# Performance work log

Hardware: AMD Instinct MI355X
Metric: run time of the kernel (lower is better)

The kernel has to match this reference:

```python
import jax, jax.numpy as jnp
import numpy as np

N_NODES = 10000
N_EDGES = 80000
F_IN = 128
H1 = 2048
H2 = 2048
H3 = 1024


def _sgconv(x, pos, src, dst, W_in, b_in, W_out, b_out):
    # geo-GCN SpatialGraphConv with hidden_size=1:
    # message(j->i) = relu(Linear(pos_j - pos_i)) * x_j ; aggr='add' ; then Linear out
    rel = pos[src] - pos[dst]                      # [E, 2]  (pos_j - pos_i)
    scale = jax.nn.relu(rel @ W_in + b_in)         # [E, C_in]
    msg = scale * x[src]                           # [E, C_in]
    agg = jax.ops.segment_sum(msg, dst, num_segments=x.shape[0])  # [N, C_in]
    return agg @ W_out + b_out                     # [N, C_out]


def setup_inputs() -> dict:
    key = jax.random.key(0)
    ks = jax.random.split(key, 12)
    x = jax.random.normal(ks[0], (N_NODES, F_IN), dtype=jnp.float32)
    pos = jax.random.normal(ks[1], (N_NODES, 2), dtype=jnp.float32)
    edge_index = jax.random.randint(ks[2], (2, N_EDGES), 0, N_NODES, dtype=jnp.int32)

    def lin(k, fan_in, fan_out):
        lim = 1.0 / np.sqrt(fan_in)
        kw, kb = jax.random.split(k)
        W = jax.random.uniform(kw, (fan_in, fan_out), jnp.float32, -lim, lim)
        b = jax.random.uniform(kb, (fan_out,), jnp.float32, -lim, lim)
        return W, b

    W_in1, b_in1 = lin(ks[3], 2, F_IN)
    W_out1, b_out1 = lin(ks[4], F_IN, H1)
    W_in2, b_in2 = lin(ks[5], 2, H1)
    W_out2, b_out2 = lin(ks[6], H1, H2)
    W_in3, b_in3 = lin(ks[7], 2, H2)
    W_out3, b_out3 = lin(ks[8], H2, H3)

    return {
        "x": x, "pos": pos, "edge_index": edge_index,
        "W_in1": W_in1, "b_in1": b_in1, "W_out1": W_out1, "b_out1": b_out1,
        "W_in2": W_in2, "b_in2": b_in2, "W_out2": W_out2, "b_out2": b_out2,
        "W_in3": W_in3, "b_in3": b_in3, "W_out3": W_out3, "b_out3": b_out3,
    }


def reference(x, pos, edge_index,
              W_in1, b_in1, W_out1, b_out1,
              W_in2, b_in2, W_out2, b_out2,
              W_in3, b_in3, W_out3, b_out3):
    src, dst = edge_index[0], edge_index[1]  # flow source_to_target: j=src, i=dst
    h = jax.nn.relu(_sgconv(x, pos, src, dst, W_in1, b_in1, W_out1, b_out1))
    h = jax.nn.relu(_sgconv(h, pos, src, dst, W_in2, b_in2, W_out2, b_out2))
    h = jax.nn.relu(_sgconv(h, pos, src, dst, W_in3, b_in3, W_out3, b_out3))
    # F.normalize(h, dim=1): L2 normalize rows with eps clamp 1e-12
    norm = jnp.linalg.norm(h, axis=1, keepdims=True)
    return h / jnp.maximum(norm, 1e-12)
```

## Files before the change

### kernel.cpp

```cpp
#include <hip/hip_runtime.h>
#include <hip/hip_bf16.h>

#define DEVI __device__ __forceinline__

constexpr int NN = 10000;
constexpr int NE = 80000;
constexpr int AGG_ROWS = 10240;

typedef __attribute__((ext_vector_type(8))) short bf16x8;
typedef __attribute__((ext_vector_type(4))) float f32x4;

DEVI float blo(unsigned int u) {
  union { unsigned int i; float f; } c; c.i = u << 16; return c.f;
}
DEVI float bhi(unsigned int u) {
  union { unsigned int i; float f; } c; c.i = u & 0xffff0000u; return c.f;
}
DEVI unsigned short f2b(float f) {
  union { float f; unsigned int i; } c; c.f = f;
  unsigned int i = c.i;
  return (unsigned short)((i + 0x7fffu + ((i >> 16) & 1u)) >> 16);
}
DEVI void st1(float* p, float v) { *p = v; }
DEVI void st1(unsigned short* p, float v) { *p = f2b(v); }
DEVI void store8b(unsigned short* p, const float v[8]) {
  int4 pk;
  pk.x = (int)((unsigned)f2b(v[0]) | ((unsigned)f2b(v[1]) << 16));
  pk.y = (int)((unsigned)f2b(v[2]) | ((unsigned)f2b(v[3]) << 16));
  pk.z = (int)((unsigned)f2b(v[4]) | ((unsigned)f2b(v[5]) << 16));
  pk.w = (int)((unsigned)f2b(v[6]) | ((unsigned)f2b(v[7]) << 16));
  *reinterpret_cast<int4*>(p) = pk;
}

DEVI void gload16(const void* g, void* l) {
  __builtin_amdgcn_global_load_lds(
      (const __attribute__((address_space(1))) void*)g,
      (__attribute__((address_space(3))) void*)l, 16, 0, 0);
}

__global__ __launch_bounds__(256)
void hist_kernel(const int* __restrict__ dst, int* __restrict__ cnt) {
  int e = blockIdx.x * 256 + threadIdx.x;
  if (e < NE) atomicAdd(&cnt[dst[e]], 1);
}

__global__ __launch_bounds__(256)
void scan_kernel(const int* __restrict__ cnt, int* __restrict__ off,
                 int* __restrict__ cursor) {
  __shared__ int buf[256];
  __shared__ int carry;
  if (threadIdx.x == 0) carry = 0;
  __syncthreads();
  for (int base = 0; base < NN; base += 256) {
    int i = base + threadIdx.x;
    int v = (i < NN) ? cnt[i] : 0;
    buf[threadIdx.x] = v;
    __syncthreads();
#pragma unroll
    for (int o = 1; o < 256; o <<= 1) {
      int t = (threadIdx.x >= o) ? buf[threadIdx.x - o] : 0;
      __syncthreads();
      buf[threadIdx.x] += t;
      __syncthreads();
    }
    int incl = buf[threadIdx.x];
    int c0 = carry;
    if (i < NN) { int ex = c0 + incl - v; off[i] = ex; cursor[i] = ex; }
    __syncthreads();
    if (threadIdx.x == 255) carry = c0 + incl;
    __syncthreads();
  }
}

__global__ __launch_bounds__(256)
void bucket_kernel(const int* __restrict__ src, const int* __restrict__ dst,
                   int* __restrict__ cursor, int* __restrict__ es) {
  int e = blockIdx.x * 256 + threadIdx.x;
  if (e < NE) {
    int p = atomicAdd(&cursor[dst[e]], 1);
    es[p] = src[e];
  }
}

__global__ __launch_bounds__(256)
void transpose_w(const float* __restrict__ W, unsigned short* __restrict__ WT,
                 int K, int N) {
  __shared__ float tile[32][33];
  int tx = threadIdx.x & 31, ty = threadIdx.x >> 5;
  int n0 = blockIdx.x * 32, k0 = blockIdx.y * 32;
#pragma unroll
  for (int j = 0; j < 32; j += 8)
    tile[ty + j][tx] = W[(size_t)(k0 + ty + j) * N + n0 + tx];
  __syncthreads();
#pragma unroll
  for (int j = 0; j < 32; j += 8)
    WT[(size_t)(n0 + ty + j) * K + k0 + tx] = f2b(tile[tx][ty + j]);
}

__global__ __launch_bounds__(256)
void gather_l1(const float* __restrict__ x, const float* __restrict__ pos,
               const int* __restrict__ off, const int* __restrict__ cnt,
               const int* __restrict__ es,
               const float* __restrict__ Win, const float* __restrict__ bin,
               unsigned short* __restrict__ agg) {
  constexpr int C = 128;
  int lane = threadIdx.x & 63;
  int i = blockIdx.x * 4 + (threadIdx.x >> 6);
  if (i >= NN) return;
  int c = lane * 2;
  float w00 = Win[c], w01 = Win[c + 1];
  float w10 = Win[C + c], w11 = Win[C + c + 1];
  float b0 = bin[c], b1 = bin[c + 1];
  float a0 = 0.f, a1 = 0.f;
  float2 pd = *reinterpret_cast<const float2*>(pos + 2 * i);
  int s0 = off[i], n = cnt[i];

  float2 r0, r1, r2, r3, q0, q1, q2, q3;
  auto ld = [&](int k, float2& r, float2& q) {
    if (k < n) {
      int s = es[s0 + k];
      float2 ps = *reinterpret_cast<const float2*>(pos + 2 * s);
      r = make_float2(ps.x - pd.x, ps.y - pd.y);
      q = *reinterpret_cast<const float2*>(x + (size_t)s * C + c);
    }
  };
  auto fma1 = [&](const float2& r, const float2& q) {
    float sc0 = fmaxf(fmaf(r.x, w00, fmaf(r.y, w10, b0)), 0.f);
    float sc1 = fmaxf(fmaf(r.x, w01, fmaf(r.y, w11, b1)), 0.f);
    a0 = fmaf(sc0, q.x, a0);
    a1 = fmaf(sc1, q.y, a1);
  };
  ld(0, r0, q0); ld(1, r1, q1); ld(2, r2, q2); ld(3, r3, q3);
  for (int k = 0; k < n; k += 4) {
    fma1(r0, q0); ld(k + 4, r0, q0);
    if (k + 1 < n) { fma1(r1, q1); } ld(k + 5, r1, q1);
    if (k + 2 < n) { fma1(r2, q2); } ld(k + 6, r2, q2);
    if (k + 3 < n) { fma1(r3, q3); } ld(k + 7, r3, q3);
  }
  unsigned int pk = (unsigned)f2b(a0) | ((unsigned)f2b(a1) << 16);
  *reinterpret_cast<unsigned int*>(agg + (size_t)i * C + c) = pk;
}

__global__ __launch_bounds__(256)
void gather_c2048(const unsigned short* __restrict__ x, const float* __restrict__ pos,
                  const int* __restrict__ off, const int* __restrict__ cnt,
                  const int* __restrict__ es,
                  const float* __restrict__ Win, const float* __restrict__ bin,
                  unsigned short* __restrict__ agg) {
  constexpr int C = 2048;
  constexpr int V = 8;
  int i = blockIdx.x;
  int c = threadIdx.x * V;
  float w0[V], w1[V], bb[V], acc[V];
#pragma unroll
  for (int j = 0; j < V; ++j) {
    w0[j] = Win[c + j]; w1[j] = Win[C + c + j]; bb[j] = bin[c + j]; acc[j] = 0.f;
  }
  float2 pd = *reinterpret_cast<const float2*>(pos + 2 * i);
  int s0 = off[i], n = cnt[i];

  float2 r0, r1, r2, r3;
  int4 q0, q1, q2, q3;
  auto ld = [&](int k, float2& r, int4& q) {
    if (k < n) {
      int s = es[s0 + k];
      float2 ps = *reinterpret_cast<const float2*>(pos + 2 * s);
      r = make_float2(ps.x - pd.x, ps.y - pd.y);
      q = *reinterpret_cast<const int4*>(x + (size_t)s * C + c);
    }
  };
  auto fma8 = [&](const float2& r, const int4& q) {
    float xv[V] = { blo(q.x), bhi(q.x), blo(q.y), bhi(q.y),
                    blo(q.z), bhi(q.z), blo(q.w), bhi(q.w) };
#pragma unroll
    for (int j = 0; j < V; ++j) {
      float sc = fmaxf(fmaf(r.x, w0[j], fmaf(r.y, w1[j], bb[j])), 0.f);
      acc[j] = fmaf(sc, xv[j], acc[j]);
    }
  };
  ld(0, r0, q0); ld(1, r1, q1); ld(2, r2, q2); ld(3, r3, q3);
  for (int k = 0; k < n; k += 4) {
    fma8(r0, q0); ld(k + 4, r0, q0);
    if (k + 1 < n) { fma8(r1, q1); } ld(k + 5, r1, q1);
    if (k + 2 < n) { fma8(r2, q2); } ld(k + 6, r2, q2);
    if (k + 3 < n) { fma8(r3, q3); } ld(k + 7, r3, q3);
  }
  store8b(agg + (size_t)i * C + c, acc);
}

template <typename OT>
__global__ __launch_bounds__(256, 2)
void gemm160(const unsigned short* __restrict__ A,
             const unsigned short* __restrict__ BT,
             const float* __restrict__ bias, OT* __restrict__ out,
             int M, int N, int K) {
  extern __shared__ unsigned short lds[];
  const int t = threadIdx.x;
  const int lane = t & 63, wid = t >> 6;
  const int wr = wid >> 1, wc = wid & 1;

  const int nwg = gridDim.x * gridDim.y;
  const int orig = blockIdx.y * gridDim.x + blockIdx.x;
  const int swz = (orig & 7) * (nwg >> 3) + (orig >> 3);
  const int bx = swz % gridDim.x, by = swz / gridDim.x;
  const int m0 = by * 160, n0 = bx * 128;
  const int nk = K >> 6;

  const int lrow = lane >> 3;
  const int schunk = (lane & 7) ^ lrow;
  const unsigned short* gA = A + (size_t)(m0 + wid * 40 + lrow) * K + schunk * 8;
  const unsigned short* gB = BT + (size_t)(n0 + wid * 32 + lrow) * K + schunk * 8;
  unsigned short* lA = lds + (wid * 5) * 512 + lane * 8;
  unsigned short* lB = lds + 20480 + (wid * 4) * 512 + lane * 8;

  auto STAGE = [&](int buf, int kt) {
    const size_t ko = (size_t)kt << 6;
#pragma unroll
    for (int jj = 0; jj < 5; ++jj)
      gload16(gA + (size_t)(jj * 8) * K + ko, lA + buf * 10240 + jj * 512);
#pragma unroll
    for (int jj = 0; jj < 4; ++jj)
      gload16(gB + (size_t)(jj * 8) * K + ko, lB + buf * 8192 + jj * 512);
  };

  const int frow = lane & 15;
  const int fr7 = frow & 7;
  const int slot0 = ((lane >> 4) ^ fr7) * 8;
  const int slot1 = ((4 + (lane >> 4)) ^ fr7) * 8;
  const int paRow = (wr * 80 + frow) * 64;
  const int pbRow = (wc * 64 + frow) * 64;

  f32x4 acc[5][4];
#pragma unroll
  for (int m = 0; m < 5; ++m)
#pragma unroll
    for (int n = 0; n < 4; ++n) acc[m][n] = 0.f;

  STAGE(0, 0);

  int cur = 0;
  for (int kt = 0; kt < nk; ++kt) {
    if (kt + 1 < nk) {
      STAGE(cur ^ 1, kt + 1);
      asm volatile("s_waitcnt vmcnt(9)" ::: "memory");
    } else {
      asm volatile("s_waitcnt vmcnt(0)" ::: "memory");
    }
    asm volatile("s_barrier" ::: "memory");
    const unsigned short* pa = lds + cur * 10240 + paRow;
    const unsigned short* pb = lds + 20480 + cur * 8192 + pbRow;
#pragma unroll
    for (int ks = 0; ks < 2; ++ks) {
      const int sl = ks ? slot1 : slot0;
      bf16x8 af[5], bf[4];
#pragma unroll
      for (int m = 0; m < 5; ++m)
        af[m] = *reinterpret_cast<const bf16x8*>(pa + m * 1024 + sl);
#pragma unroll
      for (int n = 0; n < 4; ++n)
        bf[n] = *reinterpret_cast<const bf16x8*>(pb + n * 1024 + sl);
      __builtin_amdgcn_s_setprio(1);
#pragma unroll
      for (int m = 0; m < 5; ++m)
#pragma unroll
        for (int n = 0; n < 4; ++n)
          acc[m][n] = __builtin_amdgcn_mfma_f32_16x16x32_bf16(
              af[m], bf[n], acc[m][n], 0, 0, 0);
      __builtin_amdgcn_s_setprio(0);
    }
    asm volatile("s_barrier" ::: "memory");
    cur ^= 1;
  }

  const int ccol = lane & 15;
  const int crow = (lane >> 4) * 4;
  float bv[4];
#pragma unroll
  for (int n = 0; n < 4; ++n)
    bv[n] = bias[n0 + wc * 64 + n * 16 + ccol];
#pragma unroll
  for (int m = 0; m < 5; ++m) {
    int gm0 = m0 + wr * 80 + m * 16 + crow;
#pragma unroll
    for (int r = 0; r < 4; ++r) {
      int gm = gm0 + r;
      if (gm < M) {
        size_t base = (size_t)gm * N + n0 + wc * 64 + ccol;
#pragma unroll
        for (int n = 0; n < 4; ++n)
          st1(out + base + n * 16, fmaxf(acc[m][n][r] + bv[n], 0.f));
      }
    }
  }
}

__global__ __launch_bounds__(256)
void l2norm_kernel(float* __restrict__ out) {
  constexpr int C = 1024;
  float* p = out + (size_t)blockIdx.x * C;
  float4 v = *reinterpret_cast<const float4*>(p + threadIdx.x * 4);
  float s = v.x * v.x + v.y * v.y + v.z * v.z + v.w * v.w;
#pragma unroll
  for (int o = 32; o > 0; o >>= 1) s += __shfl_down(s, o);
  __shared__ float wsum[4];
  if ((threadIdx.x & 63) == 0) wsum[threadIdx.x >> 6] = s;
  __syncthreads();
  float tot = wsum[0] + wsum[1] + wsum[2] + wsum[3];
  float inv = 1.0f / fmaxf(sqrtf(tot), 1e-12f);
  float4 r = make_float4(v.x * inv, v.y * inv, v.z * inv, v.w * inv);
  *reinterpret_cast<float4*>(p + threadIdx.x * 4) = r;
}

extern "C" void kernel_launch(void* const* d_in, const int* in_sizes, int n_in,
                              void* d_out, int out_size, void* d_ws, size_t ws_size,
                              hipStream_t stream) {
  (void)in_sizes; (void)n_in; (void)out_size; (void)ws_size;
  const float* x     = (const float*)d_in[0];
  const float* pos   = (const float*)d_in[1];
  const int*   ei    = (const int*)d_in[2];
  const int*   srcv  = ei;
  const int*   dstv  = ei + NE;
  const float* Win1  = (const float*)d_in[3];
  const float* bin1  = (const float*)d_in[4];
  const float* Wout1 = (const float*)d_in[5];
  const float* bout1 = (const float*)d_in[6];
  const float* Win2  = (const float*)d_in[7];
  const float* bin2  = (const float*)d_in[8];
  const float* Wout2 = (const float*)d_in[9];
  const float* bout2 = (const float*)d_in[10];
  const float* Win3  = (const float*)d_in[11];
  const float* bin3  = (const float*)d_in[12];
  const float* Wout3 = (const float*)d_in[13];
  const float* bout3 = (const float*)d_in[14];
  float* outp = (float*)d_out;

  char* ws = (char*)d_ws;
  unsigned short* aggb = (unsigned short*)ws;
  unsigned short* h1   = (unsigned short*)(ws + 41943040);
  unsigned short* W2T  = (unsigned short*)(ws + 82903040);
  unsigned short* W3T  = (unsigned short*)(ws + 91291648);
  unsigned short* W1T  = (unsigned short*)(ws + 95485952);
  int* cnt    = (int*)(ws + 96010240);
  int* off    = (int*)(ws + 96050240);
  int* cursor = (int*)(ws + 96090240);
  int* es     = (int*)(ws + 96130240);
  unsigned short* h2 = (unsigned short*)d_out;

  hipFuncSetAttribute((const void*)gemm160<unsigned short>,
                      hipFuncAttributeMaxDynamicSharedMemorySize, 73728);
  hipFuncSetAttribute((const void*)gemm160<float>,
                      hipFuncAttributeMaxDynamicSharedMemorySize, 73728);

  const dim3 blk(256);
  const int eb = (NE + 255) / 256;

  hipMemsetAsync(cnt, 0, NN * sizeof(int), stream);
  hist_kernel<<<eb, blk, 0, stream>>>(dstv, cnt);
  scan_kernel<<<1, blk, 0, stream>>>(cnt, off, cursor);
  bucket_kernel<<<eb, blk, 0, stream>>>(srcv, dstv, cursor, es);

  transpose_w<<<dim3(2048 / 32, 128 / 32),  blk, 0, stream>>>(Wout1, W1T, 128, 2048);
  transpose_w<<<dim3(2048 / 32, 2048 / 32), blk, 0, stream>>>(Wout2, W2T, 2048, 2048);
  transpose_w<<<dim3(1024 / 32, 2048 / 32), blk, 0, stream>>>(Wout3, W3T, 2048, 1024);

  hipMemsetAsync(aggb + (size_t)NN * 2048, 0, (size_t)(AGG_ROWS - NN) * 2048 * 2, stream);

  gather_l1<<<(NN + 3) / 4, blk, 0, stream>>>(x, pos, off, cnt, es, Win1, bin1, aggb);
  gemm160<unsigned short><<<dim3(2048 / 128, AGG_ROWS / 160), blk, 73728, stream>>>(
      aggb, W1T, bout1, h1, NN, 2048, 128);

  gather_c2048<<<NN, blk, 0, stream>>>(h1, pos, off, cnt, es, Win2, bin2, aggb);
  gemm160<unsigned short><<<dim3(2048 / 128, AGG_ROWS / 160), blk, 73728, stream>>>(
      aggb, W2T, bout2, h2, NN, 2048, 2048);

  gather_c2048<<<NN, blk, 0, stream>>>(h2, pos, off, cnt, es, Win3, bin3, aggb);
  gemm160<float><<<dim3(1024 / 128, AGG_ROWS / 160), blk, 73728, stream>>>(
      aggb, W3T, bout3, outp, NN, 1024, 2048);

  l2norm_kernel<<<NN, blk, 0, stream>>>(outp);
}
```

Baseline: 347.3 us.

## Precompute packed edge records and split wide gathers into column chunks

The bucket kernel now writes one float4 per edge holding the relative position and the source index. This removes the per-edge pos lookups and subtractions from every gather pass. The 2048-wide gathers are restructured so each wave handles one node and a 128-column chunk with 2 columns per lane, ordered so that consecutive blocks cover the same column chunk across nearby nodes. Each lane now issues 4-byte loads instead of 16-byte loads, so the wide-gather path makes many more load instructions and edge-record reads. In exchange, the grid is larger and the column-chunk working set is more L2-friendly.

```diff
diff --git a/kernel.cpp b/kernel.cpp
--- a/kernel.cpp
+++ b/kernel.cpp
@@ -23,14 +23,6 @@
 }
 DEVI void st1(float* p, float v) { *p = v; }
 DEVI void st1(unsigned short* p, float v) { *p = f2b(v); }
-DEVI void store8b(unsigned short* p, const float v[8]) {
-  int4 pk;
-  pk.x = (int)((unsigned)f2b(v[0]) | ((unsigned)f2b(v[1]) << 16));
-  pk.y = (int)((unsigned)f2b(v[2]) | ((unsigned)f2b(v[3]) << 16));
-  pk.z = (int)((unsigned)f2b(v[4]) | ((unsigned)f2b(v[5]) << 16));
-  pk.w = (int)((unsigned)f2b(v[6]) | ((unsigned)f2b(v[7]) << 16));
-  *reinterpret_cast<int4*>(p) = pk;
-}
 
 DEVI void gload16(const void* g, void* l) {
   __builtin_amdgcn_global_load_lds(
@@ -74,11 +66,15 @@
 
 __global__ __launch_bounds__(256)
 void bucket_kernel(const int* __restrict__ src, const int* __restrict__ dst,
-                   int* __restrict__ cursor, int* __restrict__ es) {
+                   const float* __restrict__ pos,
+                   int* __restrict__ cursor, float4* __restrict__ epack) {
   int e = blockIdx.x * 256 + threadIdx.x;
   if (e < NE) {
-    int p = atomicAdd(&cursor[dst[e]], 1);
-    es[p] = src[e];
+    int s = src[e], d = dst[e];
+    int p = atomicAdd(&cursor[d], 1);
+    float2 ps = *reinterpret_cast<const float2*>(pos + 2 * s);
+    float2 pd = *reinterpret_cast<const float2*>(pos + 2 * d);
+    epack[p] = make_float4(ps.x - pd.x, ps.y - pd.y, __int_as_float(s), 0.f);
   }
 }
 
@@ -98,9 +94,9 @@
 }
 
 __global__ __launch_bounds__(256)
-void gather_l1(const float* __restrict__ x, const float* __restrict__ pos,
+void gather_l1(const float* __restrict__ x,
                const int* __restrict__ off, const int* __restrict__ cnt,
-               const int* __restrict__ es,
+               const float4* __restrict__ epack,
                const float* __restrict__ Win, const float* __restrict__ bin,
                unsigned short* __restrict__ agg) {
   constexpr int C = 128;
@@ -112,80 +108,80 @@
   float w10 = Win[C + c], w11 = Win[C + c + 1];
   float b0 = bin[c], b1 = bin[c + 1];
   float a0 = 0.f, a1 = 0.f;
-  float2 pd = *reinterpret_cast<const float2*>(pos + 2 * i);
   int s0 = off[i], n = cnt[i];
 
-  float2 r0, r1, r2, r3, q0, q1, q2, q3;
-  auto ld = [&](int k, float2& r, float2& q) {
+  float4 e0, e1, e2, e3;
+  float2 q0, q1, q2, q3;
+  auto ld = [&](int k, float4& e, float2& q) {
     if (k < n) {
-      int s = es[s0 + k];
-      float2 ps = *reinterpret_cast<const float2*>(pos + 2 * s);
-      r = make_float2(ps.x - pd.x, ps.y - pd.y);
+      e = epack[s0 + k];
+      int s = __float_as_int(e.z);
       q = *reinterpret_cast<const float2*>(x + (size_t)s * C + c);
     }
   };
-  auto fma1 = [&](const float2& r, const float2& q) {
-    float sc0 = fmaxf(fmaf(r.x, w00, fmaf(r.y, w10, b0)), 0.f);
-    float sc1 = fmaxf(fmaf(r.x, w01, fmaf(r.y, w11, b1)), 0.f);
+  auto acc1 = [&](const float4& e, const float2& q) {
+    float sc0 = fmaxf(fmaf(e.x, w00, fmaf(e.y, w10, b0)), 0.f);
+    float sc1 = fmaxf(fmaf(e.x, w01, fmaf(e.y, w11, b1)), 0.f);
     a0 = fmaf(sc0, q.x, a0);
     a1 = fmaf(sc1, q.y, a1);
   };
-  ld(0, r0, q0); ld(1, r1, q1); ld(2, r2, q2); ld(3, r3, q3);
+  ld(0, e0, q0); ld(1, e1, q1); ld(2, e2, q2); ld(3, e3, q3);
   for (int k = 0; k < n; k += 4) {
-    fma1(r0, q0); ld(k + 4, r0, q0);
-    if (k + 1 < n) { fma1(r1, q1); } ld(k + 5, r1, q1);
-    if (k + 2 < n) { fma1(r2, q2); } ld(k + 6, r2, q2);
-    if (k + 3 < n) { fma1(r3, q3); } ld(k + 7, r3, q3);
+    acc1(e0, q0); ld(k + 4, e0, q0);
+    if (k + 1 < n) { acc1(e1, q1); } ld(k + 5, e1, q1);
+    if (k + 2 < n) { acc1(e2, q2); } ld(k + 6, e2, q2);
+    if (k + 3 < n) { acc1(e3, q3); } ld(k + 7, e3, q3);
   }
   unsigned int pk = (unsigned)f2b(a0) | ((unsigned)f2b(a1) << 16);
   *reinterpret_cast<unsigned int*>(agg + (size_t)i * C + c) = pk;
 }
 
 __global__ __launch_bounds__(256)
-void gather_c2048(const unsigned short* __restrict__ x, const float* __restrict__ pos,
+void gather_chunk(const unsigned short* __restrict__ x,
                   const int* __restrict__ off, const int* __restrict__ cnt,
-                  const int* __restrict__ es,
+                  const float4* __restrict__ epack,
                   const float* __restrict__ Win, const float* __restrict__ bin,
-                  unsigned short* __restrict__ agg) {
+                  unsigned short* __restrict__ agg, int ngb8) {
   constexpr int C = 2048;
-  constexpr int V = 8;
-  int i = blockIdx.x;
-  int c = threadIdx.x * V;
-  float w0[V], w1[V], bb[V], acc[V];
-#pragma unroll
-  for (int j = 0; j < V; ++j) {
-    w0[j] = Win[c + j]; w1[j] = Win[C + c + j]; bb[j] = bin[c + j]; acc[j] = 0.f;
-  }
-  float2 pd = *reinterpret_cast<const float2*>(pos + 2 * i);
+  int wgid = blockIdx.x;
+  int half = wgid >= ngb8;
+  int base = half ? wgid - ngb8 : wgid;
+  int chunk = (base & 7) + (half << 3);
+  int grp = base >> 3;
+  int lane = threadIdx.x & 63;
+  int i = grp * 4 + (threadIdx.x >> 6);
+  if (i >= NN) return;
+  int c = chunk * 128 + lane * 2;
+  float w00 = Win[c], w01 = Win[c + 1];
+  float w10 = Win[C + c], w11 = Win[C + c + 1];
+  float b0 = bin[c], b1 = bin[c + 1];
+  float a0 = 0.f, a1 = 0.f;
   int s0 = off[i], n = cnt[i];
 
-  float2 r0, r1, r2, r3;
-  int4 q0, q1, q2, q3;
-  auto ld = [&](int k, float2& r, int4& q) {
+  float4 e0, e1, e2, e3;
+  unsigned int q0, q1, q2, q3;
+  auto ld = [&](int k, float4& e, unsigned int& q) {
     if (k < n) {
-      int s = es[s0 + k];
-      float2 ps = *reinterpret_cast<const float2*>(pos + 2 * s);
-      r = make_float2(ps.x - pd.x, ps.y - pd.y);
-      q = *reinterpret_cast<const int4*>(x + (size_t)s * C + c);
-    }
-  };
-  auto fma8 = [&](const float2& r, const int4& q) {
-    float xv[V] = { blo(q.x), bhi(q.x), blo(q.y), bhi(q.y),
-                    blo(q.z), bhi(q.z), blo(q.w), bhi(q.w) };
-#pragma unroll
-    for (int j = 0; j < V; ++j) {
-      float sc = fmaxf(fmaf(r.x, w0[j], fmaf(r.y, w1[j], bb[j])), 0.f);
-      acc[j] = fmaf(sc, xv[j], acc[j]);
-    }
-  };
-  ld(0, r0, q0); ld(1, r1, q1); ld(2, r2, q2); ld(3, r3, q3);
+      e = epack[s0 + k];
+      int s = __float_as_int(e.z);
+      q = *reinterpret_cast<const unsigned int*>(x + (size_t)s * C + c);
+    }
+  };
+  auto acc1 = [&](const float4& e, unsigned int q) {
+    float sc0 = fmaxf(fmaf(e.x, w00, fmaf(e.y, w10, b0)), 0.f);
+    float sc1 = fmaxf(fmaf(e.x, w01, fmaf(e.y, w11, b1)), 0.f);
+    a0 = fmaf(sc0, blo(q), a0);
+    a1 = fmaf(sc1, bhi(q), a1);
+  };
+  ld(0, e0, q0); ld(1, e1, q1); ld(2, e2, q2); ld(3, e3, q3);
   for (int k = 0; k < n; k += 4) {
-    fma8(r0, q0); ld(k + 4, r0, q0);
-    if (k + 1 < n) { fma8(r1, q1); } ld(k + 5, r1, q1);
-    if (k + 2 < n) { fma8(r2, q2); } ld(k + 6, r2, q2);
-    if (k + 3 < n) { fma8(r3, q3); } ld(k + 7, r3, q3);
-  }
-  store8b(agg + (size_t)i * C + c, acc);
+    acc1(e0, q0); ld(k + 4, e0, q0);
+    if (k + 1 < n) { acc1(e1, q1); } ld(k + 5, e1, q1);
+    if (k + 2 < n) { acc1(e2, q2); } ld(k + 6, e2, q2);
+    if (k + 3 < n) { acc1(e3, q3); } ld(k + 7, e3, q3);
+  }
+  unsigned int pk = (unsigned)f2b(a0) | ((unsigned)f2b(a1) << 16);
+  *reinterpret_cast<unsigned int*>(agg + (size_t)i * C + c) = pk;
 }
 
 template <typename OT>
@@ -343,7 +339,7 @@
   int* cnt    = (int*)(ws + 96010240);
   int* off    = (int*)(ws + 96050240);
   int* cursor = (int*)(ws + 96090240);
-  int* es     = (int*)(ws + 96130240);
+  float4* epack = (float4*)(ws + 96130240);
   unsigned short* h2 = (unsigned short*)d_out;
 
   hipFuncSetAttribute((const void*)gemm160<unsigned short>,
@@ -353,11 +349,12 @@
 
   const dim3 blk(256);
   const int eb = (NE + 255) / 256;
+  const int ngb8 = ((NN + 3) / 4) * 8;
 
   hipMemsetAsync(cnt, 0, NN * sizeof(int), stream);
   hist_kernel<<<eb, blk, 0, stream>>>(dstv, cnt);
   scan_kernel<<<1, blk, 0, stream>>>(cnt, off, cursor);
-  bucket_kernel<<<eb, blk, 0, stream>>>(srcv, dstv, cursor, es);
+  bucket_kernel<<<eb, blk, 0, stream>>>(srcv, dstv, pos, cursor, epack);
 
   transpose_w<<<dim3(2048 / 32, 128 / 32),  blk, 0, stream>>>(Wout1, W1T, 128, 2048);
   transpose_w<<<dim3(2048 / 32, 2048 / 32), blk, 0, stream>>>(Wout2, W2T, 2048, 2048);
@@ -365,15 +362,15 @@
 
   hipMemsetAsync(aggb + (size_t)NN * 2048, 0, (size_t)(AGG_ROWS - NN) * 2048 * 2, stream);
 
-  gather_l1<<<(NN + 3) / 4, blk, 0, stream>>>(x, pos, off, cnt, es, Win1, bin1, aggb);
+  gather_l1<<<(NN + 3) / 4, blk, 0, stream>>>(x, off, cnt, epack, Win1, bin1, aggb);
   gemm160<unsigned short><<<dim3(2048 / 128, AGG_ROWS / 160), blk, 73728, stream>>>(
       aggb, W1T, bout1, h1, NN, 2048, 128);
 
-  gather_c2048<<<NN, blk, 0, stream>>>(h1, pos, off, cnt, es, Win2, bin2, aggb);
+  gather_chunk<<<2 * ngb8, blk, 0, stream>>>(h1, off, cnt, epack, Win2, bin2, aggb, ngb8);
   gemm160<unsigned short><<<dim3(2048 / 128, AGG_ROWS / 160), blk, 73728, stream>>>(
       aggb, W2T, bout2, h2, NN, 2048, 2048);
 
-  gather_c2048<<<NN, blk, 0, stream>>>(h2, pos, off, cnt, es, Win3, bin3, aggb);
+  gather_chunk<<<2 * ngb8, blk, 0, stream>>>(h2, off, cnt, epack, Win3, bin3, aggb, ngb8);
   gemm160<float><<<dim3(1024 / 128, AGG_ROWS / 160), blk, 73728, stream>>>(
       aggb, W3T, bout3, outp, NN, 1024, 2048);
 
```

New measurement: 432.7 us. 24.6% more time.
